# Kernel tuning notes

Hardware: AMD Instinct MI355X
Metric: run time of the kernel (lower is better)

The kernel has to match this reference:

```python
import jax, jax.numpy as jnp
import numpy as np

B, N, K = 2, 8192, 16
C_IN, C_OUT, HID = 64, 256, 256
L, HEADS, DKQV = 2, 8, 32
D = HEADS * DKQV  # 256


def setup_inputs() -> dict:
    key = jax.random.key(0)
    ks = jax.random.split(key, 20)
    s = 0.02
    inp = {
        "xyzs": jax.random.normal(ks[0], (B, N, 3), jnp.float32),
        "features": jax.random.normal(ks[1], (B, N, C_IN), jnp.float32),
        "k_graph": jax.random.randint(ks[2], (B, N, K), 0, N),
        "W_in": jax.random.normal(ks[3], (C_IN, HID), jnp.float32) * s,
        "b_in": jnp.zeros((HID,), jnp.float32),
        "Wq": jax.random.normal(ks[4], (L, HID, D), jnp.float32) * s,
        "bq": jnp.zeros((L, D), jnp.float32),
        "Wk": jax.random.normal(ks[5], (L, HID, D), jnp.float32) * s,
        "bk": jnp.zeros((L, D), jnp.float32),
        "Wv": jax.random.normal(ks[6], (L, HID, D), jnp.float32) * s,
        "bv": jnp.zeros((L, D), jnp.float32),
        "Wp": jax.random.normal(ks[7], (L, 3, D), jnp.float32) * s,
        "bp": jnp.zeros((L, D), jnp.float32),
        "Wo": jax.random.normal(ks[8], (L, D, HID), jnp.float32) * s,
        "bo": jnp.zeros((L, HID), jnp.float32),
        "W_out": jax.random.normal(ks[9], (HID, C_OUT), jnp.float32) * s,
        "b_out": jnp.zeros((C_OUT,), jnp.float32),
    }
    return inp


def _gather(f, idx):
    # f: [B,N,D], idx: [B,N,K] -> [B,N,K,D]
    return jnp.take_along_axis(f[:, None], idx[..., None], axis=2)


def _knn_attn(xyz, f, idx, Wq, bq, Wk, bk, Wv, bv, Wp, bp, Wo, bo):
    b, n, _ = f.shape
    q = f @ Wq + bq                      # [B,N,D]
    k = f @ Wk + bk
    v = f @ Wv + bv
    k_nb = _gather(k, idx)               # [B,N,K,D]
    v_nb = _gather(v, idx)
    rel = xyz[:, :, None, :] - _gather(xyz, idx)   # [B,N,K,3]
    pos = rel @ Wp + bp                  # [B,N,K,D] relative positional encoding
    kh = (k_nb + pos).reshape(b, n, K, HEADS, DKQV)
    vh = (v_nb + pos).reshape(b, n, K, HEADS, DKQV)
    qh = q.reshape(b, n, HEADS, DKQV)
    logits = jnp.einsum('bnhd,bnkhd->bnhk', qh, kh) / np.sqrt(DKQV)
    attn = jax.nn.softmax(logits, axis=-1)          # softmax over K neighbors
    o = jnp.einsum('bnhk,bnkhd->bnhd', attn, vh).reshape(b, n, D)
    return o @ Wo + bo


def reference(xyzs, features, k_graph, W_in, b_in, Wq, bq, Wk, bk, Wv, bv,
              Wp, bp, Wo, bo, W_out, b_out):
    f = features @ W_in + b_in
    for l in range(L):
        res = f  # res_connection=True
        f = _knn_attn(xyzs, f, k_graph, Wq[l], bq[l], Wk[l], bk[l],
                      Wv[l], bv[l], Wp[l], bp[l], Wo[l], bo[l]) + res
    out = f @ W_out + b_out
    return jax.nn.leaky_relu(out, negative_slope=0.01)
```

## Files before the change

kernel.cpp:

```cpp
#include <hip/hip_runtime.h>
#include <hip/hip_bf16.h>

typedef __attribute__((ext_vector_type(8))) short bf16x8;
typedef __attribute__((ext_vector_type(4))) float f32x4;
typedef __attribute__((ext_vector_type(2))) _Float16 h2;
typedef __attribute__((ext_vector_type(8))) _Float16 h8;
typedef unsigned int uint;

constexpr int NPTS = 8192;
constexpr int BPTS = 16384;
constexpr int KNN  = 16;

__device__ __forceinline__ void gload16(const void* g, void* l) {
    __builtin_amdgcn_global_load_lds(
        (const __attribute__((address_space(1))) unsigned int*)g,
        (__attribute__((address_space(3))) unsigned int*)l, 16, 0, 0);
}

template<int KD, bool RES, int OUTT, bool LRELU, int BM = 128>
__global__ __launch_bounds__(256) void gemm_mfma(
    const __hip_bfloat16* __restrict__ A,
    const __hip_bfloat16* __restrict__ Bt,
    const float* __restrict__ b0, const float* __restrict__ b1,
    const float* __restrict__ b2,
    const __hip_bfloat16* __restrict__ res,
    void* __restrict__ Cout, int M, int N)
{
    constexpr int WM = BM / 2;
    constexpr int MI = WM / 16;

    __shared__ __align__(16) __hip_bfloat16 As[BM * 64];
    __shared__ __align__(16) __hip_bfloat16 Bs[128 * 64];

    const int tid  = threadIdx.x;
    const int lane = tid & 63;
    const int wid  = tid >> 6;
    const int wm   = (wid >> 1) * WM;
    const int wn   = (wid & 1) * 64;
    const int bm   = blockIdx.y * BM;
    const int bn   = blockIdx.x * 128;

    const int srow8 = lane >> 3;
    const int sslot = (lane & 7) ^ srow8;
    const int r = lane & 15;
    const int g = lane >> 4;

    f32x4 acc[MI][4] = {};

    for (int k0 = 0; k0 < KD; k0 += 64) {
        #pragma unroll
        for (int p = 0; p < BM / 32; ++p) {
            const int rowA = p * 32 + wid * 8 + srow8;
            gload16(&A[(size_t)(bm + rowA) * KD + k0 + sslot * 8],
                    (char*)As + (p * 32 + wid * 8) * 128);
        }
        #pragma unroll
        for (int p = 0; p < 4; ++p) {
            const int rowB = p * 32 + wid * 8 + srow8;
            gload16(&Bt[(size_t)(bn + rowB) * KD + k0 + sslot * 8],
                    (char*)Bs + (p * 32 + wid * 8) * 128);
        }
        __syncthreads();

        bf16x8 af[2][MI], bfr[2][4];
        #pragma unroll
        for (int s = 0; s < 2; ++s) {
            const int physA = (s * 4 + g) ^ (r & 7);
            #pragma unroll
            for (int mi = 0; mi < MI; ++mi)
                af[s][mi] = *(const bf16x8*)((const char*)As + (wm + mi * 16 + r) * 128 + physA * 16);
            #pragma unroll
            for (int ni = 0; ni < 4; ++ni)
                bfr[s][ni] = *(const bf16x8*)((const char*)Bs + (wn + ni * 16 + r) * 128 + physA * 16);
        }
        #pragma unroll
        for (int s = 0; s < 2; ++s)
            #pragma unroll
            for (int mi = 0; mi < MI; ++mi)
                #pragma unroll
                for (int ni = 0; ni < 4; ++ni)
                    acc[mi][ni] = __builtin_amdgcn_mfma_f32_16x16x32_bf16(
                        af[s][mi], bfr[s][ni], acc[mi][ni], 0, 0, 0);
        __syncthreads();
    }

    #pragma unroll
    for (int ni = 0; ni < 4; ++ni) {
        const int col = bn + wn + ni * 16 + r;
        const float* bsel = (col < 256) ? b0 : (col < 512 ? b1 : b2);
        const float bias = bsel[col & 255];
        #pragma unroll
        for (int mi = 0; mi < MI; ++mi) {
            #pragma unroll
            for (int q = 0; q < 4; ++q) {
                const int row = bm + wm + mi * 16 + g * 4 + q;
                float v = acc[mi][ni][q] + bias;
                if (RES)  v += __bfloat162float(res[(size_t)row * N + col]);
                if (LRELU) v = v > 0.f ? v : 0.01f * v;
                if (OUTT == 0)      ((float*)Cout)[(size_t)row * N + col] = v;
                else if (OUTT == 1) ((__hip_bfloat16*)Cout)[(size_t)row * N + col] = __float2bfloat16(v);
                else                ((_Float16*)Cout)[(size_t)row * N + col] = (_Float16)v;
            }
        }
    }
}

__global__ __launch_bounds__(256) void prep_kernel(
    const float* __restrict__ W_in, const float* __restrict__ Wq,
    const float* __restrict__ Wk,  const float* __restrict__ Wv,
    const float* __restrict__ Wo,  const float* __restrict__ W_out,
    const float* __restrict__ features,
    const float* __restrict__ Wp,  const float* __restrict__ bp,
    __hip_bfloat16* __restrict__ WtIn,  __hip_bfloat16* __restrict__ WtQKV,
    __hip_bfloat16* __restrict__ WtO,   __hip_bfloat16* __restrict__ WtOut,
    __hip_bfloat16* __restrict__ featb, _Float16* __restrict__ Wpb)
{
    const int b = blockIdx.x;
    if (b < 592) {
        const float* srcs[10] = {W_in, Wq, Wk, Wv, Wq + 65536, Wk + 65536,
                                 Wv + 65536, Wo, Wo + 65536, W_out};
        __hip_bfloat16* dsts[10] = {
            WtIn, WtQKV, WtQKV + 65536, WtQKV + 131072,
            WtQKV + 196608, WtQKV + 262144, WtQKV + 327680,
            WtO, WtO + 65536, WtOut};
        const int Ks[10]    = {64,256,256,256,256,256,256,256,256,256};
        const int start[10] = {0,16,80,144,208,272,336,400,464,528};
        int j = 0;
        #pragma unroll
        for (int i = 1; i < 10; ++i) if (b >= start[i]) j = i;
        const int t  = b - start[j];
        const int Kd = Ks[j];
        const int ntk = Kd >> 5;
        const int tn = t / ntk;
        const int tk = t - tn * ntk;

        __shared__ float s[32][33];
        const int tx = threadIdx.x & 31, ty = threadIdx.x >> 5;
        const float* src = srcs[j];
        #pragma unroll
        for (int i = 0; i < 4; ++i)
            s[ty + i * 8][tx] = src[(size_t)(tk * 32 + ty + i * 8) * 256 + tn * 32 + tx];
        __syncthreads();
        __hip_bfloat16* dst = dsts[j];
        #pragma unroll
        for (int i = 0; i < 4; ++i)
            dst[(size_t)(tn * 32 + ty + i * 8) * Kd + tk * 32 + tx] =
                __float2bfloat16(s[tx][ty + i * 8]);
    } else if (b < 1616) {
        const int i = (b - 592) * 1024 + threadIdx.x * 4;
        const float4 v = *(const float4*)&features[i];
        __hip_bfloat16 tmp[4] = {__float2bfloat16(v.x), __float2bfloat16(v.y),
                                 __float2bfloat16(v.z), __float2bfloat16(v.w)};
        *(uint2*)&featb[i] = *(const uint2*)tmp;
    } else {
        const int e8 = threadIdx.x * 8;
        const int l  = e8 >> 10;
        const int rr = (e8 >> 8) & 3;
        const int c  = e8 & 255;
        const float* src = (rr < 3) ? (Wp + (size_t)l * 768 + rr * 256 + c)
                                    : (bp + (size_t)l * 256 + c);
        const float4 f0 = ((const float4*)src)[0];
        const float4 f1 = ((const float4*)src)[1];
        _Float16 t[8] = {(_Float16)f0.x, (_Float16)f0.y, (_Float16)f0.z, (_Float16)f0.w,
                         (_Float16)f1.x, (_Float16)f1.y, (_Float16)f1.z, (_Float16)f1.w};
        *(uint4*)&Wpb[(size_t)l * 1024 + rr * 256 + c] = *(const uint4*)t;
    }
}

__global__ __launch_bounds__(256) void knn_attn_kernel(
    const float* __restrict__ xyz,
    const int*   __restrict__ idx,
    const _Float16* __restrict__ qkv,
    const _Float16* __restrict__ Wpb,
    __hip_bfloat16* __restrict__ o)
{
    const int tid = threadIdx.x;
    const int pt  = tid >> 7;
    const int lt  = tid & 127;
    const int p0  = blockIdx.x * 2;
    const int p   = p0 + pt;
    const int hh  = lt >> 4;
    const int k   = lt & 15;

    __shared__ float s_rel[2][KNN][3];
    __shared__ float s_wq[2][8][4];
    __shared__ _Float16 s_ah[2][8][KNN];
    __shared__ float s_arel[2][8][3];
    __shared__ __align__(16) char v_raw[16384];

    const int jrow = ((p >> 13) << 13) + idx[p * KNN + k];
    const h8* qp = (const h8*)(qkv + (size_t)p * 768 + hh * 32);
    const h8* kp = (const h8*)(qkv + (size_t)jrow * 768 + 256 + hh * 32);
    const h8 q0 = qp[0], q1 = qp[1];
    const h8 k0 = kp[0], k1 = kp[1];

    const int sk = lt >> 3;
    const int c4 = lt & 7;
    const int jr_st = ((p >> 13) << 13) + idx[p * KNN + sk];
    const uint4* vsrc = (const uint4*)(qkv + (size_t)jr_st * 768 + 512 + c4 * 8);
    const uint4 st0 = vsrc[0];
    const uint4 st1 = vsrc[8];
    const uint4 st2 = vsrc[16];
    const uint4 st3 = vsrc[24];
    const int dbase = pt * 8192 + (sk >> 2) * 2048 + (c4 >> 1) * 128
                    + (sk & 3) * 32 + (c4 & 1) * 16;

    if (tid < 32) {
        const int pp = tid >> 4, kk = tid & 15;
        const int pg = p0 + pp;
        const int jr = ((pg >> 13) << 13) + idx[pg * KNN + kk];
        s_rel[pp][kk][0] = xyz[pg * 3 + 0] - xyz[jr * 3 + 0];
        s_rel[pp][kk][1] = xyz[pg * 3 + 1] - xyz[jr * 3 + 1];
        s_rel[pp][kk][2] = xyz[pg * 3 + 2] - xyz[jr * 3 + 2];
    } else if (tid < 96) {
        const int t2 = tid - 32;
        const int pp = t2 >> 5, hq = (t2 >> 2) & 7, j = t2 & 3;
        const h8* qr = (const h8*)(qkv + (size_t)(p0 + pp) * 768 + hq * 32);
        const h8* wr = (const h8*)(Wpb + j * 256 + hq * 32);
        const h8 a0 = qr[0], a1 = qr[1], b0 = wr[0], b1 = wr[1];
        float acc = 0.f;
        #pragma unroll
        for (int i = 0; i < 4; ++i)
            acc = __builtin_amdgcn_fdot2(((const h2*)&a0)[i], ((const h2*)&b0)[i], acc, false);
        #pragma unroll
        for (int i = 0; i < 4; ++i)
            acc = __builtin_amdgcn_fdot2(((const h2*)&a1)[i], ((const h2*)&b1)[i], acc, false);
        s_wq[pp][hq][j] = acc;
    }

    float dot = 0.f;
    #pragma unroll
    for (int i = 0; i < 4; ++i)
        dot = __builtin_amdgcn_fdot2(((const h2*)&q0)[i], ((const h2*)&k0)[i], dot, false);
    #pragma unroll
    for (int i = 0; i < 4; ++i)
        dot = __builtin_amdgcn_fdot2(((const h2*)&q1)[i], ((const h2*)&k1)[i], dot, false);
    __syncthreads();

    const float r0 = s_rel[pt][k][0], r1 = s_rel[pt][k][1], r2 = s_rel[pt][k][2];
    const float logit = (dot + r0 * s_wq[pt][hh][0] + r1 * s_wq[pt][hh][1]
                             + r2 * s_wq[pt][hh][2] + s_wq[pt][hh][3])
                        * 0.1767766952966369f;
    float mx = logit;
    #pragma unroll
    for (int off = 8; off >= 1; off >>= 1)
        mx = fmaxf(mx, __shfl_xor(mx, off, 16));
    const float e = __expf(logit - mx);
    float den = e;
    #pragma unroll
    for (int off = 8; off >= 1; off >>= 1)
        den += __shfl_xor(den, off, 16);
    const float attn = e / den;
    s_ah[pt][hh][k] = (_Float16)attn;

    float a0 = attn * r0, a1 = attn * r1, a2 = attn * r2;
    #pragma unroll
    for (int off = 8; off >= 1; off >>= 1) {
        a0 += __shfl_xor(a0, off, 16);
        a1 += __shfl_xor(a1, off, 16);
        a2 += __shfl_xor(a2, off, 16);
    }
    if (k == 0) {
        s_arel[pt][hh][0] = a0;
        s_arel[pt][hh][1] = a1;
        s_arel[pt][hh][2] = a2;
    }

    *(uint4*)(v_raw + dbase +    0) = st0;
    *(uint4*)(v_raw + dbase +  512) = st1;
    *(uint4*)(v_raw + dbase + 1024) = st2;
    *(uint4*)(v_raw + dbase + 1536) = st3;
    __syncthreads();

    {
        const int w   = tid >> 6;
        const int l   = tid & 63;
        const int pt2 = w >> 1;
        const int H   = w & 1;
        const int g   = l >> 4;
        const int li  = l & 15;
        const int chA = H * 128 + g * 16 + li;
        const int chB = chA + 64;
        const int hA  = chA >> 5, hB = chB >> 5;
        const int p2  = p0 + pt2;

        const unsigned vg = (unsigned)(size_t)
            (__attribute__((address_space(3))) char*)(v_raw + pt2 * 8192 + H * 1024 + l * 8);

        uint2 rA0, rA1, rA2, rA3, rB0, rB1, rB2, rB3;
        asm volatile("ds_read_b64_tr_b16 %0, %1 offset:0"    : "=v"(rA0) : "v"(vg));
        asm volatile("ds_read_b64_tr_b16 %0, %1 offset:2048" : "=v"(rA1) : "v"(vg));
        asm volatile("ds_read_b64_tr_b16 %0, %1 offset:4096" : "=v"(rA2) : "v"(vg));
        asm volatile("ds_read_b64_tr_b16 %0, %1 offset:6144" : "=v"(rA3) : "v"(vg));
        asm volatile("ds_read_b64_tr_b16 %0, %1 offset:512"  : "=v"(rB0) : "v"(vg));
        asm volatile("ds_read_b64_tr_b16 %0, %1 offset:2560" : "=v"(rB1) : "v"(vg));
        asm volatile("ds_read_b64_tr_b16 %0, %1 offset:4608" : "=v"(rB2) : "v"(vg));
        asm volatile("ds_read_b64_tr_b16 %0, %1 offset:6656" : "=v"(rB3) : "v"(vg));
        asm volatile("s_waitcnt lgkmcnt(0)" ::: "memory");
        __builtin_amdgcn_sched_barrier(0);

        const h2* aA = (const h2*)&s_ah[pt2][hA][0];
        const h2* aB = (const h2*)&s_ah[pt2][hB][0];

        float oA = 0.f, oB = 0.f;
        #define PVKT(rr, aa, acc, kt)                                             \
            acc = __builtin_amdgcn_fdot2(aa[2*kt],   *(const h2*)&rr.x, acc, false); \
            acc = __builtin_amdgcn_fdot2(aa[2*kt+1], *(const h2*)&rr.y, acc, false);
        PVKT(rA0, aA, oA, 0) PVKT(rA1, aA, oA, 1) PVKT(rA2, aA, oA, 2) PVKT(rA3, aA, oA, 3)
        PVKT(rB0, aB, oB, 0) PVKT(rB1, aB, oB, 1) PVKT(rB2, aB, oB, 2) PVKT(rB3, aB, oB, 3)
        #undef PVKT

        const float gA0 = s_arel[pt2][hA][0], gA1 = s_arel[pt2][hA][1], gA2 = s_arel[pt2][hA][2];
        const float gB0 = s_arel[pt2][hB][0], gB1 = s_arel[pt2][hB][1], gB2 = s_arel[pt2][hB][2];
        oA += gA0 * (float)Wpb[chA] + gA1 * (float)Wpb[256 + chA]
            + gA2 * (float)Wpb[512 + chA] + (float)Wpb[768 + chA];
        oB += gB0 * (float)Wpb[chB] + gB1 * (float)Wpb[256 + chB]
            + gB2 * (float)Wpb[512 + chB] + (float)Wpb[768 + chB];
        o[(size_t)p2 * 256 + chA] = __float2bfloat16(oA);
        o[(size_t)p2 * 256 + chB] = __float2bfloat16(oB);
    }
}

extern "C" void kernel_launch(void* const* d_in, const int* in_sizes, int n_in,
                              void* d_out, int out_size, void* d_ws, size_t ws_size,
                              hipStream_t stream)
{
    const float* xyzs     = (const float*)d_in[0];
    const float* features = (const float*)d_in[1];
    const int*   k_graph  = (const int*)  d_in[2];
    const float* W_in     = (const float*)d_in[3];
    const float* b_in     = (const float*)d_in[4];
    const float* Wq       = (const float*)d_in[5];
    const float* bq       = (const float*)d_in[6];
    const float* Wk       = (const float*)d_in[7];
    const float* bk       = (const float*)d_in[8];
    const float* Wv       = (const float*)d_in[9];
    const float* bv       = (const float*)d_in[10];
    const float* Wp       = (const float*)d_in[11];
    const float* bp       = (const float*)d_in[12];
    const float* Wo       = (const float*)d_in[13];
    const float* bo       = (const float*)d_in[14];
    const float* W_out    = (const float*)d_in[15];
    const float* b_out    = (const float*)d_in[16];

    __hip_bfloat16* featb = (__hip_bfloat16*)d_ws;
    __hip_bfloat16* f     = featb + 1048576;
    _Float16*       qkv   = (_Float16*)(f + 4194304);
    __hip_bfloat16* ob    = (__hip_bfloat16*)(qkv + 12582912);
    __hip_bfloat16* WtIn  = ob + 4194304;
    __hip_bfloat16* WtQKV = WtIn + 16384;
    __hip_bfloat16* WtO   = WtQKV + 393216;
    __hip_bfloat16* WtOut = WtO + 131072;
    _Float16*       Wpb   = (_Float16*)(WtOut + 65536);

    prep_kernel<<<1617, 256, 0, stream>>>(W_in, Wq, Wk, Wv, Wo, W_out, features,
                                          Wp, bp, WtIn, WtQKV, WtO, WtOut,
                                          featb, Wpb);

    gemm_mfma<64, false, 1, false, 64><<<dim3(2, 256), 256, 0, stream>>>(
        featb, WtIn, b_in, b_in, b_in, nullptr, f, BPTS, 256);

    for (int l = 0; l < 2; ++l) {
        gemm_mfma<256, false, 2, false, 128><<<dim3(6, 128), 256, 0, stream>>>(
            f, WtQKV + (size_t)l * 196608,
            bq + l * 256, bk + l * 256, bv + l * 256, nullptr, qkv, BPTS, 768);

        knn_attn_kernel<<<dim3(BPTS / 2), 256, 0, stream>>>(
            xyzs, k_graph, qkv, Wpb + (size_t)l * 1024, ob);

        gemm_mfma<256, true, 1, false, 64><<<dim3(2, 256), 256, 0, stream>>>(
            ob, WtO + (size_t)l * 65536,
            bo + l * 256, bo + l * 256, bo + l * 256, f, f, BPTS, 256);
    }

    gemm_mfma<256, false, 0, true, 64><<<dim3(2, 256), 256, 0, stream>>>(
        f, WtOut, b_out, b_out, b_out, nullptr, (float*)d_out, BPTS, 256);
}
```

Baseline: 128.1 us.

## Fold input projection into layer-0 QKV weights and fuse both GEMMs

Precomputes W_in·Wq/Wk/Wv and the matching combined biases in the prep kernel, so layer 0's QKV projection can be computed straight from the 64-channel input features. A single GEMM with K=64 and N=1024 now writes both f (bf16) and layer-0 qkv (fp16), which removes the separate K=256 QKV GEMM for layer 0 and one re-read of f. The cost is extra prep work, a tiny fp32 weight-product computation, and slightly different rounding because the fused weights are quantized to bf16.

```diff
diff --git a/kernel.cpp b/kernel.cpp
--- a/kernel.cpp
+++ b/kernel.cpp
@@ -22,9 +22,10 @@
     const __hip_bfloat16* __restrict__ A,
     const __hip_bfloat16* __restrict__ Bt,
     const float* __restrict__ b0, const float* __restrict__ b1,
-    const float* __restrict__ b2,
+    const float* __restrict__ b2, const float* __restrict__ b3,
     const __hip_bfloat16* __restrict__ res,
-    void* __restrict__ Cout, int M, int N)
+    void* __restrict__ Cout, int M, int N,
+    void* __restrict__ Cout2)
 {
     constexpr int WM = BM / 2;
     constexpr int MI = WM / 16;
@@ -87,8 +88,14 @@
     #pragma unroll
     for (int ni = 0; ni < 4; ++ni) {
         const int col = bn + wn + ni * 16 + r;
-        const float* bsel = (col < 256) ? b0 : (col < 512 ? b1 : b2);
-        const float bias = bsel[col & 255];
+        float bias;
+        if (OUTT == 4) {
+            const float* barr[4] = {b0, b1, b2, b3};
+            bias = barr[col >> 8][col & 255];
+        } else {
+            const float* bsel = (col < 256) ? b0 : (col < 512 ? b1 : b2);
+            bias = bsel[col & 255];
+        }
         #pragma unroll
         for (int mi = 0; mi < MI; ++mi) {
             #pragma unroll
@@ -99,7 +106,13 @@
                 if (LRELU) v = v > 0.f ? v : 0.01f * v;
                 if (OUTT == 0)      ((float*)Cout)[(size_t)row * N + col] = v;
                 else if (OUTT == 1) ((__hip_bfloat16*)Cout)[(size_t)row * N + col] = __float2bfloat16(v);
-                else                ((_Float16*)Cout)[(size_t)row * N + col] = (_Float16)v;
+                else if (OUTT == 2) ((_Float16*)Cout)[(size_t)row * N + col] = (_Float16)v;
+                else {
+                    if (col < 256)
+                        ((__hip_bfloat16*)Cout)[(size_t)row * 256 + col] = __float2bfloat16(v);
+                    else
+                        ((_Float16*)Cout2)[(size_t)row * 768 + col - 256] = (_Float16)v;
+                }
             }
         }
     }
@@ -111,16 +124,22 @@
     const float* __restrict__ Wo,  const float* __restrict__ W_out,
     const float* __restrict__ features,
     const float* __restrict__ Wp,  const float* __restrict__ bp,
-    __hip_bfloat16* __restrict__ WtIn,  __hip_bfloat16* __restrict__ WtQKV,
+    const float* __restrict__ b_in,
+    const float* __restrict__ bq,  const float* __restrict__ bk,
+    const float* __restrict__ bv,
+    __hip_bfloat16* __restrict__ Wcomb,
+    __hip_bfloat16* __restrict__ WtQKV,
     __hip_bfloat16* __restrict__ WtO,   __hip_bfloat16* __restrict__ WtOut,
-    __hip_bfloat16* __restrict__ featb, _Float16* __restrict__ Wpb)
+    __hip_bfloat16* __restrict__ featb, _Float16* __restrict__ Wpb,
+    float* __restrict__ bc)
 {
+    __shared__ __align__(16) float smem[4096];
     const int b = blockIdx.x;
     if (b < 592) {
         const float* srcs[10] = {W_in, Wq, Wk, Wv, Wq + 65536, Wk + 65536,
                                  Wv + 65536, Wo, Wo + 65536, W_out};
         __hip_bfloat16* dsts[10] = {
-            WtIn, WtQKV, WtQKV + 65536, WtQKV + 131072,
+            Wcomb, WtQKV, WtQKV + 65536, WtQKV + 131072,
             WtQKV + 196608, WtQKV + 262144, WtQKV + 327680,
             WtO, WtO + 65536, WtOut};
         const int Ks[10]    = {64,256,256,256,256,256,256,256,256,256};
@@ -134,7 +153,7 @@
         const int tn = t / ntk;
         const int tk = t - tn * ntk;
 
-        __shared__ float s[32][33];
+        float (*s)[33] = (float(*)[33])smem;
         const int tx = threadIdx.x & 31, ty = threadIdx.x >> 5;
         const float* src = srcs[j];
         #pragma unroll
@@ -152,7 +171,7 @@
         __hip_bfloat16 tmp[4] = {__float2bfloat16(v.x), __float2bfloat16(v.y),
                                  __float2bfloat16(v.z), __float2bfloat16(v.w)};
         *(uint2*)&featb[i] = *(const uint2*)tmp;
-    } else {
+    } else if (b == 1616) {
         const int e8 = threadIdx.x * 8;
         const int l  = e8 >> 10;
         const int rr = (e8 >> 8) & 3;
@@ -164,6 +183,40 @@
         _Float16 t[8] = {(_Float16)f0.x, (_Float16)f0.y, (_Float16)f0.z, (_Float16)f0.w,
                          (_Float16)f1.x, (_Float16)f1.y, (_Float16)f1.z, (_Float16)f1.w};
         *(uint4*)&Wpb[(size_t)l * 1024 + rr * 256 + c] = *(const uint4*)t;
+    } else {
+        float (*ws)[16] = (float(*)[16])smem;
+        const int c0  = (b - 1617) * 16;
+        const int seg = c0 >> 8;
+        const int cs  = c0 & 255;
+        const float* Wsrc = seg == 0 ? Wq : (seg == 1 ? Wk : Wv);
+        const float* bsrc = seg == 0 ? bq : (seg == 1 ? bk : bv);
+        const int tx = threadIdx.x & 15, ty = threadIdx.x >> 4;
+
+        #pragma unroll 4
+        for (int i = 0; i < 16; ++i)
+            ws[ty + i * 16][tx] = Wsrc[(size_t)(ty + i * 16) * 256 + cs + tx];
+        __syncthreads();
+
+        #pragma unroll
+        for (int j = 0; j < 4; ++j) {
+            const int rr = ty + j * 16;
+            float acc = 0.f;
+            for (int k = 0; k < 256; k += 4) {
+                const float4 w = *(const float4*)&W_in[(size_t)rr * 256 + k];
+                acc += w.x * ws[k][tx] + w.y * ws[k + 1][tx]
+                     + w.z * ws[k + 2][tx] + w.w * ws[k + 3][tx];
+            }
+            Wcomb[(size_t)(256 + c0 + tx) * 64 + rr] = __float2bfloat16(acc);
+        }
+        if (ty == 0) {
+            float acc = 0.f;
+            for (int k = 0; k < 256; k += 4) {
+                const float4 w = *(const float4*)&b_in[k];
+                acc += w.x * ws[k][tx] + w.y * ws[k + 1][tx]
+                     + w.z * ws[k + 2][tx] + w.w * ws[k + 3][tx];
+            }
+            bc[c0 + tx] = acc + bsrc[cs + tx];
+        }
     }
 }
 
@@ -347,32 +400,36 @@
     __hip_bfloat16* f     = featb + 1048576;
     _Float16*       qkv   = (_Float16*)(f + 4194304);
     __hip_bfloat16* ob    = (__hip_bfloat16*)(qkv + 12582912);
-    __hip_bfloat16* WtIn  = ob + 4194304;
-    __hip_bfloat16* WtQKV = WtIn + 16384;
+    __hip_bfloat16* Wcomb = ob + 4194304;
+    __hip_bfloat16* WtQKV = Wcomb + 65536;
     __hip_bfloat16* WtO   = WtQKV + 393216;
     __hip_bfloat16* WtOut = WtO + 131072;
     _Float16*       Wpb   = (_Float16*)(WtOut + 65536);
-
-    prep_kernel<<<1617, 256, 0, stream>>>(W_in, Wq, Wk, Wv, Wo, W_out, features,
-                                          Wp, bp, WtIn, WtQKV, WtO, WtOut,
-                                          featb, Wpb);
-
-    gemm_mfma<64, false, 1, false, 64><<<dim3(2, 256), 256, 0, stream>>>(
-        featb, WtIn, b_in, b_in, b_in, nullptr, f, BPTS, 256);
+    float*          bc    = (float*)(Wpb + 2048);
+
+    prep_kernel<<<1665, 256, 0, stream>>>(W_in, Wq, Wk, Wv, Wo, W_out, features,
+                                          Wp, bp, b_in, bq, bk, bv,
+                                          Wcomb, WtQKV, WtO, WtOut,
+                                          featb, Wpb, bc);
+
+    gemm_mfma<64, false, 4, false, 64><<<dim3(8, 256), 256, 0, stream>>>(
+        featb, Wcomb, b_in, bc, bc + 256, bc + 512, nullptr, f, BPTS, 1024, qkv);
 
     for (int l = 0; l < 2; ++l) {
-        gemm_mfma<256, false, 2, false, 128><<<dim3(6, 128), 256, 0, stream>>>(
-            f, WtQKV + (size_t)l * 196608,
-            bq + l * 256, bk + l * 256, bv + l * 256, nullptr, qkv, BPTS, 768);
+        if (l == 1) {
+            gemm_mfma<256, false, 2, false, 128><<<dim3(6, 128), 256, 0, stream>>>(
+                f, WtQKV + 196608,
+                bq + 256, bk + 256, bv + 256, nullptr, nullptr, qkv, BPTS, 768, nullptr);
+        }
 
         knn_attn_kernel<<<dim3(BPTS / 2), 256, 0, stream>>>(
             xyzs, k_graph, qkv, Wpb + (size_t)l * 1024, ob);
 
         gemm_mfma<256, true, 1, false, 64><<<dim3(2, 256), 256, 0, stream>>>(
             ob, WtO + (size_t)l * 65536,
-            bo + l * 256, bo + l * 256, bo + l * 256, f, f, BPTS, 256);
+            bo + l * 256, bo + l * 256, bo + l * 256, nullptr, f, f, BPTS, 256, nullptr);
     }
 
     gemm_mfma<256, false, 0, true, 64><<<dim3(2, 256), 256, 0, stream>>>(
-        f, WtOut, b_out, b_out, b_out, nullptr, (float*)d_out, BPTS, 256);
+        f, WtOut, b_out, b_out, b_out, nullptr, nullptr, (float*)d_out, BPTS, 256, nullptr);
 }
```

Measured after the change: 140.2 us. +9.4%, slower.
